# Kernel tuning notes

Measured on AMD Instinct MI355X. Metric: run time of the kernel, lower is better.

Reference implementation:

```python
import jax, jax.numpy as jnp
import numpy as np

NEG_SLOPE = 0.2


def setup_inputs() -> dict:
    key = jax.random.key(0)
    k1, k2, k3 = jax.random.split(key, 3)
    B, N, IN, OUT, C = 2048, 256, 256, 256, 1024
    x = jax.random.normal(k1, (B, N, IN), dtype=jnp.float32)
    indices = jax.random.randint(k2, (B,), 0, C)
    # kaiming-uniform-like init for weight
    bound = float(np.sqrt(6.0 / IN))
    weight = jax.random.uniform(k3, (C, IN, OUT), dtype=jnp.float32, minval=-bound, maxval=bound)
    bias = jnp.zeros((1, 1, OUT), dtype=jnp.float32)
    return {"x": x, "indices": indices, "weight": weight, "bias": bias}


def reference(x, indices, weight, bias):
    # gather per-batch weight tiles: [B, IN, OUT], then batched matmul
    w = weight[indices]                      # [B, IN, OUT]
    out = jnp.einsum('bni,bio->bno', x, w)   # [B, N, OUT]
    out = out + bias[0]                      # bias[0] is [1, OUT], broadcasts
    return jnp.where(out >= 0, out, NEG_SLOPE * out)  # LeakyReLU(0.2)
```

## Files before the change

### kernel.cpp

```cpp
#include <hip/hip_runtime.h>
#include <hip/hip_bf16.h>


#define N_DIM 256
#define K_DIM 256
#define O_DIM 256
#define BK 32

typedef __attribute__((ext_vector_type(8))) __bf16 bf16x8;
typedef __attribute__((ext_vector_type(4))) float f32x4;
typedef __attribute__((ext_vector_type(4))) unsigned int u32x4;
typedef __attribute__((ext_vector_type(2))) unsigned int u32x2;

__device__ __forceinline__ f32x4 MFMA(u32x4 a, u32x4 b, f32x4 c) {
    return __builtin_amdgcn_mfma_f32_16x16x32_bf16(
        __builtin_bit_cast(bf16x8, a), __builtin_bit_cast(bf16x8, b), c, 0, 0, 0);
}

__device__ __forceinline__ unsigned pk2(float a, float b) {
    __hip_bfloat16 ha = __float2bfloat16(a);
    __hip_bfloat16 hb = __float2bfloat16(b);
    unsigned short sa, sb;
    __builtin_memcpy(&sa, &ha, 2);
    __builtin_memcpy(&sb, &hb, 2);
    return (unsigned)sa | ((unsigned)sb << 16);
}

__device__ __forceinline__ int swz(int row, int k) {
    const int rp = row >> 1;
    const int ch = (((row & 1) << 2) + (k >> 3)) ^ (rp & 7);
    return rp * 128 + ch * 16 + (k & 7) * 2;
}

__global__ __launch_bounds__(256) void argemm_kernel(
    const float* __restrict__ x,
    const int* __restrict__ idx,
    const float* __restrict__ w,
    const float* __restrict__ bias,
    float* __restrict__ out)
{
    __shared__ __align__(16) char lds[49152];

    const int tid = threadIdx.x;
    const int l   = tid & 63;
    const int wid = tid >> 6;
    const int wr  = wid >> 1;
    const int wc  = wid & 1;

    const unsigned bid     = blockIdx.x;
    const unsigned chunk   = gridDim.x >> 3;
    const unsigned logical = (bid & 7u) * chunk + (bid >> 3);
    const int b    = (int)(logical >> 2);
    const int tpos = (int)(logical & 3u);
    const int n0   = (tpos >> 1) * 128;
    const int o0   = (tpos & 1) * 128;

    const int c = idx[b];
    const float* xb = x + (size_t)b * (N_DIM * K_DIM);
    const float* wb = w + (size_t)c * (K_DIM * O_DIM);

    const int lr3 = l >> 3, kc = l & 7;
    int gA[4], aW[4];
#pragma unroll
    for (int q = 0; q < 4; ++q) {
        const int rA = wid * 32 + q * 8 + lr3;
        gA[q] = (n0 + rA) * K_DIM + kc * 4;
        aW[q] = swz(rA, kc * 4);
    }
    const int kq = tid >> 5;
    const int m4 = (tid & 31) * 4;
    int gB[4], bW[4];
#pragma unroll
    for (int dk = 0; dk < 4; ++dk)
        gB[dk] = (kq * 4 + dk) * O_DIM + o0 + m4;
#pragma unroll
    for (int j = 0; j < 4; ++j)
        bW[j] = swz(m4 + j, kq * 4);

    const int g = l >> 4;
    const int i = l & 15;
    int aR[4], bR[4];
#pragma unroll
    for (int m = 0; m < 4; ++m) aR[m] = swz(wr * 64 + m * 16 + i, g * 8);
#pragma unroll
    for (int n = 0; n < 4; ++n) bR[n] = 8192 + swz(wc * 64 + n * 16 + i, g * 8);

    f32x4 ra[2][4], rb[2][4];

    auto issue = [&](int t, int s) {
#pragma unroll
        for (int q = 0; q < 4; ++q)
            ra[s][q] = *(const f32x4*)(xb + gA[q] + t * BK);
#pragma unroll
        for (int dk = 0; dk < 4; ++dk)
            rb[s][dk] = *(const f32x4*)(wb + gB[dk] + t * (BK * O_DIM));
    };
    auto flush = [&](int t, int s) {
        char* base = (char*)lds + (t % 3) * 16384;
#pragma unroll
        for (int q = 0; q < 4; ++q) {
            u32x2 p;
            p.x = pk2(ra[s][q].x, ra[s][q].y);
            p.y = pk2(ra[s][q].z, ra[s][q].w);
            *(u32x2*)(base + aW[q]) = p;
        }
#pragma unroll
        for (int j = 0; j < 4; ++j) {
            u32x2 p;
            p.x = pk2(rb[s][0][j], rb[s][1][j]);
            p.y = pk2(rb[s][2][j], rb[s][3][j]);
            *(u32x2*)(base + 8192 + bW[j]) = p;
        }
    };

    f32x4 acc[4][4];
#pragma unroll
    for (int m = 0; m < 4; ++m)
#pragma unroll
        for (int n = 0; n < 4; ++n)
            acc[m][n] = (f32x4){0.f, 0.f, 0.f, 0.f};

    issue(0, 0);
    __builtin_amdgcn_sched_barrier(0);
    issue(1, 1);
    __builtin_amdgcn_sched_barrier(0);
    flush(0, 0);
    issue(2, 0);
    __builtin_amdgcn_sched_barrier(0);
    asm volatile("s_waitcnt lgkmcnt(0)" ::: "memory");
    __builtin_amdgcn_sched_barrier(0);
    __builtin_amdgcn_s_barrier();

#pragma unroll
    for (int t = 0; t < 8; ++t) {
        const char* base = (const char*)lds + (t % 3) * 16384;

        u32x4 af[4];
#pragma unroll
        for (int m = 0; m < 4; ++m)
            af[m] = *(const u32x4*)(base + aR[m]);
#pragma unroll
        for (int n = 0; n < 4; ++n) {
            const u32x4 bq = *(const u32x4*)(base + bR[n]);
#pragma unroll
            for (int m = 0; m < 4; ++m)
                acc[m][n] = MFMA(af[m], bq, acc[m][n]);
        }

        if (t < 7) {
            flush(t + 1, (t + 1) & 1);
            if (t < 5) {
                issue(t + 3, (t + 1) & 1);
                __builtin_amdgcn_sched_barrier(0);
            }
            asm volatile("s_waitcnt lgkmcnt(0)" ::: "memory");
            __builtin_amdgcn_sched_barrier(0);
            __builtin_amdgcn_s_barrier();
        }
    }

    float biasf[4];
#pragma unroll
    for (int n = 0; n < 4; ++n)
        biasf[n] = bias[o0 + wc * 64 + n * 16 + i];

    float* ob = out + (size_t)b * (N_DIM * O_DIM);
#pragma unroll
    for (int m = 0; m < 4; ++m) {
#pragma unroll
        for (int r = 0; r < 4; ++r) {
            const int row = n0 + wr * 64 + m * 16 + g * 4 + r;
#pragma unroll
            for (int n = 0; n < 4; ++n) {
                float v = acc[m][n][r] + biasf[n];
                v = (v >= 0.f) ? v : 0.2f * v;
                ob[row * O_DIM + o0 + wc * 64 + n * 16 + i] = v;
            }
        }
    }
}

extern "C" void kernel_launch(void* const* d_in, const int* in_sizes, int n_in,
                              void* d_out, int out_size, void* d_ws, size_t ws_size,
                              hipStream_t stream) {
    const float* x    = (const float*)d_in[0];
    const int*   idx  = (const int*)d_in[1];
    const float* w    = (const float*)d_in[2];
    const float* bias = (const float*)d_in[3];
    float*       out  = (float*)d_out;
    (void)d_ws; (void)ws_size; (void)n_in; (void)out_size;

    const int B = in_sizes[1];
    dim3 grid((unsigned)(B * 4)), block(256);
    hipLaunchKernelGGL(argemm_kernel, grid, block, 0, stream, x, idx, w, bias, out);
}
```

Baseline: 298.3 us.

## Retile to 32-row blocks with A fragments held in registers

Each block now computes 32 rows by the full 256 output columns instead of a 128x128 tile, which doubles the grid. Each thread loads its whole A (x) fragment straight from global memory into registers as bf16, so only the weight tile is staged through LDS, with a new swizzle and 16-byte writes. Launch bounds now request 3 blocks per SM to raise occupancy. The trade-off is that each block re-reads the full weight slice, giving 8 reads of it per batch instead of 2. The x loads are also strided scalar reads rather than vector loads.

```diff
diff --git a/kernel.cpp b/kernel.cpp
--- a/kernel.cpp
+++ b/kernel.cpp
@@ -2,15 +2,12 @@
 #include <hip/hip_bf16.h>
 
 
-#define N_DIM 256
 #define K_DIM 256
 #define O_DIM 256
-#define BK 32
 
 typedef __attribute__((ext_vector_type(8))) __bf16 bf16x8;
 typedef __attribute__((ext_vector_type(4))) float f32x4;
 typedef __attribute__((ext_vector_type(4))) unsigned int u32x4;
-typedef __attribute__((ext_vector_type(2))) unsigned int u32x2;
 
 __device__ __forceinline__ f32x4 MFMA(u32x4 a, u32x4 b, f32x4 c) {
     return __builtin_amdgcn_mfma_f32_16x16x32_bf16(
@@ -26,13 +23,14 @@
     return (unsigned)sa | ((unsigned)sb << 16);
 }
 
-__device__ __forceinline__ int swz(int row, int k) {
-    const int rp = row >> 1;
-    const int ch = (((row & 1) << 2) + (k >> 3)) ^ (rp & 7);
-    return rp * 128 + ch * 16 + (k & 7) * 2;
+__device__ __forceinline__ int bbyte(int o, int p) {
+    const int rp  = o >> 1;
+    const int raw = ((o & 1) << 2) | (p >> 3);
+    const int key = (rp ^ (o >> 4)) & 7;
+    return rp * 128 + ((raw ^ key) << 4) + ((p & 7) << 1);
 }
 
-__global__ __launch_bounds__(256) void argemm_kernel(
+__global__ __launch_bounds__(256, 3) void argemm_kernel(
     const float* __restrict__ x,
     const int* __restrict__ idx,
     const float* __restrict__ w,
@@ -50,107 +48,98 @@
     const unsigned bid     = blockIdx.x;
     const unsigned chunk   = gridDim.x >> 3;
     const unsigned logical = (bid & 7u) * chunk + (bid >> 3);
-    const int b    = (int)(logical >> 2);
-    const int tpos = (int)(logical & 3u);
-    const int n0   = (tpos >> 1) * 128;
-    const int o0   = (tpos & 1) * 128;
-
-    const int c = idx[b];
-    const float* xb = x + (size_t)b * (N_DIM * K_DIM);
-    const float* wb = w + (size_t)c * (K_DIM * O_DIM);
-
-    const int lr3 = l >> 3, kc = l & 7;
-    int gA[4], aW[4];
-#pragma unroll
-    for (int q = 0; q < 4; ++q) {
-        const int rA = wid * 32 + q * 8 + lr3;
-        gA[q] = (n0 + rA) * K_DIM + kc * 4;
-        aW[q] = swz(rA, kc * 4);
-    }
-    const int kq = tid >> 5;
-    const int m4 = (tid & 31) * 4;
-    int gB[4], bW[4];
-#pragma unroll
-    for (int dk = 0; dk < 4; ++dk)
-        gB[dk] = (kq * 4 + dk) * O_DIM + o0 + m4;
-#pragma unroll
-    for (int j = 0; j < 4; ++j)
-        bW[j] = swz(m4 + j, kq * 4);
+    const int b  = (int)(logical >> 3);
+    const int n0 = (int)(logical & 7u) * 32;
 
     const int g = l >> 4;
     const int i = l & 15;
-    int aR[4], bR[4];
+
+    const int c = idx[b];
+    const float* xb = x + (size_t)b * (256 * 256);
+    const float* wb = w + (size_t)c * (256 * 256);
+
+    const float* wp = wb + l * 4;
+    int bW[4];
 #pragma unroll
-    for (int m = 0; m < 4; ++m) aR[m] = swz(wr * 64 + m * 16 + i, g * 8);
+    for (int j = 0; j < 4; ++j)
+        bW[j] = bbyte(l * 4 + j, wid * 8);
+
+    int bR[8];
 #pragma unroll
-    for (int n = 0; n < 4; ++n) bR[n] = 8192 + swz(wc * 64 + n * 16 + i, g * 8);
+    for (int n = 0; n < 8; ++n)
+        bR[n] = bbyte(wc * 128 + n * 16 + i, g * 8);
 
-    f32x4 ra[2][4], rb[2][4];
+    f32x4 rb[2][8];
 
-    auto issue = [&](int t, int s) {
+    auto issueB = [&](int t, int s) {
 #pragma unroll
-        for (int q = 0; q < 4; ++q)
-            ra[s][q] = *(const f32x4*)(xb + gA[q] + t * BK);
-#pragma unroll
-        for (int dk = 0; dk < 4; ++dk)
-            rb[s][dk] = *(const f32x4*)(wb + gB[dk] + t * (BK * O_DIM));
+        for (int q = 0; q < 8; ++q)
+            rb[s][q] = *(const f32x4*)(wp + (size_t)(t * 32 + q * 4 + wid) * 256);
     };
-    auto flush = [&](int t, int s) {
-        char* base = (char*)lds + (t % 3) * 16384;
-#pragma unroll
-        for (int q = 0; q < 4; ++q) {
-            u32x2 p;
-            p.x = pk2(ra[s][q].x, ra[s][q].y);
-            p.y = pk2(ra[s][q].z, ra[s][q].w);
-            *(u32x2*)(base + aW[q]) = p;
-        }
+    auto flushB = [&](int T, int s) {
+        char* d = (char*)lds + (T % 3) * 16384;
 #pragma unroll
         for (int j = 0; j < 4; ++j) {
-            u32x2 p;
+            u32x4 p;
             p.x = pk2(rb[s][0][j], rb[s][1][j]);
             p.y = pk2(rb[s][2][j], rb[s][3][j]);
-            *(u32x2*)(base + 8192 + bW[j]) = p;
+            p.z = pk2(rb[s][4][j], rb[s][5][j]);
+            p.w = pk2(rb[s][6][j], rb[s][7][j]);
+            *(u32x4*)(d + bW[j]) = p;
         }
     };
 
-    f32x4 acc[4][4];
+    issueB(0, 0);
+    __builtin_amdgcn_sched_barrier(0);
+    issueB(1, 1);
+    __builtin_amdgcn_sched_barrier(0);
+
+    const float* xrow = xb + (n0 + wr * 16 + i) * 256 + g;
+    u32x4 af[8];
 #pragma unroll
-    for (int m = 0; m < 4; ++m)
+    for (int tb = 0; tb < 2; ++tb) {
+        float av[4][8];
 #pragma unroll
-        for (int n = 0; n < 4; ++n)
-            acc[m][n] = (f32x4){0.f, 0.f, 0.f, 0.f};
+        for (int t4 = 0; t4 < 4; ++t4)
+#pragma unroll
+            for (int s = 0; s < 8; ++s)
+                av[t4][s] = xrow[(tb * 4 + t4) * 32 + s * 4];
+#pragma unroll
+        for (int t4 = 0; t4 < 4; ++t4) {
+            u32x4 a;
+            a.x = pk2(av[t4][0], av[t4][1]);
+            a.y = pk2(av[t4][2], av[t4][3]);
+            a.z = pk2(av[t4][4], av[t4][5]);
+            a.w = pk2(av[t4][6], av[t4][7]);
+            af[tb * 4 + t4] = a;
+        }
+    }
 
-    issue(0, 0);
-    __builtin_amdgcn_sched_barrier(0);
-    issue(1, 1);
-    __builtin_amdgcn_sched_barrier(0);
-    flush(0, 0);
-    issue(2, 0);
+    flushB(0, 0);
+    issueB(2, 0);
     __builtin_amdgcn_sched_barrier(0);
     asm volatile("s_waitcnt lgkmcnt(0)" ::: "memory");
     __builtin_amdgcn_sched_barrier(0);
     __builtin_amdgcn_s_barrier();
 
+    f32x4 acc[8];
+#pragma unroll
+    for (int n = 0; n < 8; ++n)
+        acc[n] = (f32x4){0.f, 0.f, 0.f, 0.f};
+
 #pragma unroll
     for (int t = 0; t < 8; ++t) {
-        const char* base = (const char*)lds + (t % 3) * 16384;
-
-        u32x4 af[4];
+        const char* buf = (const char*)lds + (t % 3) * 16384;
 #pragma unroll
-        for (int m = 0; m < 4; ++m)
-            af[m] = *(const u32x4*)(base + aR[m]);
-#pragma unroll
-        for (int n = 0; n < 4; ++n) {
-            const u32x4 bq = *(const u32x4*)(base + bR[n]);
-#pragma unroll
-            for (int m = 0; m < 4; ++m)
-                acc[m][n] = MFMA(af[m], bq, acc[m][n]);
+        for (int n = 0; n < 8; ++n) {
+            const u32x4 bq = *(const u32x4*)(buf + bR[n]);
+            acc[n] = MFMA(af[t], bq, acc[n]);
         }
 
         if (t < 7) {
-            flush(t + 1, (t + 1) & 1);
+            flushB(t + 1, (t + 1) & 1);
             if (t < 5) {
-                issue(t + 3, (t + 1) & 1);
+                issueB(t + 3, (t + 1) & 1);
                 __builtin_amdgcn_sched_barrier(0);
             }
             asm volatile("s_waitcnt lgkmcnt(0)" ::: "memory");
@@ -159,23 +148,20 @@
         }
     }
 
-    float biasf[4];
+    float biasf[8];
 #pragma unroll
-    for (int n = 0; n < 4; ++n)
-        biasf[n] = bias[o0 + wc * 64 + n * 16 + i];
+    for (int n = 0; n < 8; ++n)
+        biasf[n] = bias[wc * 128 + n * 16 + i];
 
-    float* ob = out + (size_t)b * (N_DIM * O_DIM);
+    float* ob = out + (size_t)b * (256 * 256);
 #pragma unroll
-    for (int m = 0; m < 4; ++m) {
+    for (int n = 0; n < 8; ++n) {
 #pragma unroll
         for (int r = 0; r < 4; ++r) {
-            const int row = n0 + wr * 64 + m * 16 + g * 4 + r;
-#pragma unroll
-            for (int n = 0; n < 4; ++n) {
-                float v = acc[m][n][r] + biasf[n];
-                v = (v >= 0.f) ? v : 0.2f * v;
-                ob[row * O_DIM + o0 + wc * 64 + n * 16 + i] = v;
-            }
+            const int row = n0 + wr * 16 + g * 4 + r;
+            float v = acc[n][r] + biasf[n];
+            v = (v >= 0.f) ? v : 0.2f * v;
+            ob[row * 256 + wc * 128 + n * 16 + i] = v;
         }
     }
 }
@@ -191,6 +177,6 @@
     (void)d_ws; (void)ws_size; (void)n_in; (void)out_size;
 
     const int B = in_sizes[1];
-    dim3 grid((unsigned)(B * 4)), block(256);
+    dim3 grid((unsigned)(B * 8)), block(256);
     hipLaunchKernelGGL(argemm_kernel, grid, block, 0, stream, x, idx, w, bias, out);
 }
```

After: 717.3 us. 140% more time.
